# Kernel tuning notes

Measured on AMD Instinct MI355X. Metric: run time of the kernel, lower is better.

## Reference

```python
import jax, jax.numpy as jnp
import numpy as np

B, T, D, HS = 4, 4096, 1024, 64

def setup_inputs() -> dict:
    key = jax.random.key(0)
    kx, kq, kk, kv = jax.random.split(key, 4)
    s = 1.0 / np.sqrt(D)  # torch Linear default-ish init scale
    return {
        "x": jax.random.normal(kx, (B, T, D), dtype=jnp.float32),
        "Wq": jax.random.uniform(kq, (D, HS), jnp.float32, -s, s),
        "Wk": jax.random.uniform(kk, (D, HS), jnp.float32, -s, s),
        "Wv": jax.random.uniform(kv, (D, HS), jnp.float32, -s, s),
    }

def reference(x, Wq, Wk, Wv):
    # x: [B,T,D]; Wq/Wk/Wv: [D,HS]
    q = jnp.einsum('btd,dh->bth', x, Wq)
    k = jnp.einsum('btd,dh->bth', x, Wk)
    v = jnp.einsum('btd,dh->bth', x, Wv)
    # NOTE: source scales by C**-0.5 with C = d_model (input dim), not head_size
    scale = jnp.asarray(D, x.dtype) ** -0.5
    weights = jnp.einsum('bqh,bkh->bqk', q, k) * scale  # [B,T,T]
    weights = jax.nn.softmax(weights, axis=-1)
    out = jnp.einsum('bqk,bkh->bqh', weights, v)  # [B,T,HS]
    return out
```

## Files before the change

kernel.cpp:

```cpp
#include <hip/hip_runtime.h>


typedef __bf16 bf16;
typedef __bf16 bf16x4 __attribute__((ext_vector_type(4)));
typedef __bf16 bf16x8 __attribute__((ext_vector_type(8)));
typedef float  f32x16 __attribute__((ext_vector_type(16)));

#define MFMA(a, b, c) __builtin_amdgcn_mfma_f32_32x32x16_bf16(a, b, c, 0, 0, 0)

constexpr int T = 4096, D = 1024, HS = 64;
constexpr int ROWS = 4 * T;
constexpr float QSCL = 0.045084220027797f;

__device__ __forceinline__ void gld16(const void* g, void* l) {
    __builtin_amdgcn_global_load_lds(
        (const __attribute__((address_space(1))) unsigned int*)g,
        (__attribute__((address_space(3))) unsigned int*)l, 16, 0, 0);
}

__device__ inline f32x16 zero16() {
    f32x16 z;
#pragma unroll
    for (int i = 0; i < 16; ++i) z[i] = 0.f;
    return z;
}

__global__ __launch_bounds__(256) void prep_wt(
    const float* __restrict__ Wq, const float* __restrict__ Wk,
    const float* __restrict__ Wv, bf16* __restrict__ Wt)
{
    __shared__ float Xf[64 * 68];
    const int m = blockIdx.x >> 4, dt = blockIdx.x & 15;
    const float* W = (m == 0) ? Wq : ((m == 1) ? Wk : Wv);
    const int d0 = dt * 64;
#pragma unroll
    for (int j = 0; j < 4; ++j) {
        int i = threadIdx.x + 256 * j;
        int dr = i >> 4, c4 = i & 15;
        float4 v = *(const float4*)(W + (size_t)(d0 + dr) * 64 + c4 * 4);
        *(float4*)&Xf[dr * 68 + c4 * 4] = v;
    }
    __syncthreads();
    const float scl = (m == 0) ? QSCL : 1.0f;
#pragma unroll
    for (int j = 0; j < 4; ++j) {
        int o = threadIdx.x + 256 * j;
        int h = o >> 4, dc = o & 15;
        bf16x4 w;
#pragma unroll
        for (int k = 0; k < 4; ++k) w[k] = (bf16)(Xf[(dc * 4 + k) * 68 + h] * scl);
        *(bf16x4*)(Wt + (size_t)(m * 64 + h) * D + d0 + dc * 4) = w;
    }
}

__global__ __launch_bounds__(256) void qkv_proj(
    const float* __restrict__ x, const bf16* __restrict__ Wt,
    bf16* __restrict__ Qg, bf16* __restrict__ Kgt, bf16* __restrict__ Vgt)
{
    __shared__ __align__(16) bf16  Xb[2][64 * 64];
    __shared__ __align__(16) short Ws[2][192 * 64];
    const int tid = threadIdx.x;
    const int w = tid >> 6, lane = tid & 63, ln5 = lane & 31, hi = lane >> 5;
    const int tt = w & 1, hh = w >> 1;
    const int xcd = blockIdx.x & 7, mlocal = blockIdx.x >> 3;
    const int r0 = (xcd * 32 + mlocal) * 64;
    const int wb = tid & 448;

    auto stageW = [&](int kc, int buf) {
#pragma unroll
        for (int k2 = 0; k2 < 6; ++k2) {
            int s = k2 * 256 + tid;
            int h = s >> 3, j = s & 7, u = j ^ (h & 7);
            gld16(Wt + (size_t)h * D + kc * 64 + u * 8,
                  &Ws[buf][(k2 * 256 + wb) * 8]);
        }
    };
    float4 xra[2], xrb[2];
    auto stageX_load = [&](int kc) {
#pragma unroll
        for (int k = 0; k < 2; ++k) {
            int e = k * 256 + tid;
            int r = e >> 3, d0 = (e & 7) * 8;
            const float* src = x + (size_t)(r0 + r) * D + kc * 64 + d0;
            xra[k] = *(const float4*)src;
            xrb[k] = *(const float4*)(src + 4);
        }
    };
    auto stageX_write = [&](int buf) {
#pragma unroll
        for (int k = 0; k < 2; ++k) {
            int e = k * 256 + tid;
            int r = e >> 3, d0 = (e & 7) * 8;
            bf16x8 v;
            v[0] = (bf16)xra[k].x; v[1] = (bf16)xra[k].y;
            v[2] = (bf16)xra[k].z; v[3] = (bf16)xra[k].w;
            v[4] = (bf16)xrb[k].x; v[5] = (bf16)xrb[k].y;
            v[6] = (bf16)xrb[k].z; v[7] = (bf16)xrb[k].w;
            *(bf16x8*)&Xb[buf][r * 64 + (((d0 >> 3) ^ (r & 7)) * 8)] = v;
        }
    };

    f32x16 acc0 = zero16(), acc1 = zero16(), acc2 = zero16();
    const int rx = tt * 32 + ln5;
    const int hq = hh * 32 + ln5;
    const int swz = ln5 & 7;

    stageX_load(0); stageW(0, 0); stageX_write(0);
    __syncthreads();
    for (int kc = 0; kc < 16; ++kc) {
        const int cur = kc & 1;
        if (kc < 15) { stageW(kc + 1, cur ^ 1); stageX_load(kc + 1); }
        const bf16*  Xc = &Xb[cur][0];
        const short* Wb = &Ws[cur][0];
#pragma unroll
        for (int ks = 0; ks < 4; ++ks) {
            int g = (ks * 2 + hi) ^ swz;
            bf16x8 fx = *(const bf16x8*)&Xc[rx * 64 + g * 8];
            bf16x8 w0 = *(const bf16x8*)&Wb[(hq)       * 64 + g * 8];
            bf16x8 w1 = *(const bf16x8*)&Wb[(64 + hq)  * 64 + g * 8];
            bf16x8 w2 = *(const bf16x8*)&Wb[(128 + hq) * 64 + g * 8];
            acc0 = MFMA(w0, fx, acc0);
            acc1 = MFMA(w1, fx, acc1);
            acc2 = MFMA(fx, w2, acc2);
        }
        if (kc < 15) stageX_write(cur ^ 1);
        __syncthreads();
    }

    {
        int t = r0 + tt * 32 + ln5;
#pragma unroll
        for (int g = 0; g < 4; ++g) {
            int h0 = hh * 32 + 8 * g + 4 * hi;
            bf16x4 v;
#pragma unroll
            for (int k = 0; k < 4; ++k) v[k] = (bf16)acc0[4 * g + k];
            *(bf16x4*)(Qg + (size_t)t * HS + h0) = v;
        }
    }
    {
        int t = r0 + tt * 32 + ln5;
#pragma unroll
        for (int g = 0; g < 4; ++g) {
            int h0 = hh * 32 + 8 * g + 4 * hi;
            bf16x4 v;
#pragma unroll
            for (int k = 0; k < 4; ++k) v[k] = (bf16)acc1[4 * g + k];
            int j = (h0 >> 3) ^ (t & 7);
            *(bf16x4*)(Kgt + (size_t)t * HS + j * 8 + 4 * hi) = v;
        }
    }
    {
        int hr = hh * 32 + ln5;
#pragma unroll
        for (int g = 0; g < 4; ++g) {
            int t0 = tt * 32 + 8 * g + 4 * hi;
            bf16x4 v;
#pragma unroll
            for (int k = 0; k < 4; ++k) v[k] = (bf16)acc2[4 * g + k];
            int j = (t0 >> 3) ^ (hr & 7);
            *(bf16x4*)(Vgt + (size_t)r0 * HS + hr * 64 + j * 8 + 4 * hi) = v;
        }
    }
}

__global__ __launch_bounds__(256, 2) void attn(
    const bf16* __restrict__ Qg, const bf16* __restrict__ Kgt,
    const bf16* __restrict__ Vgt, float* __restrict__ Op,
    float* __restrict__ Lp, float* __restrict__ out, int split)
{
    __shared__ __align__(16) short PO[16384];
    __shared__ float Lx[128];

    const int tid = threadIdx.x;
    const int w = tid >> 6, lane = tid & 63, ln5 = lane & 31, hi = lane >> 5;
    const int wq = w & 1, wk = w >> 1;

    int b, qt, half;
    if (split == 4) {
        int rest = blockIdx.x >> 3; qt = rest & 31;
        int combo = (blockIdx.x & 7) + 8 * (rest >> 5);
        b = combo >> 2; half = combo & 3;
    } else if (split == 2) {
        int c2 = blockIdx.x & 7; b = c2 >> 1; half = c2 & 1; qt = blockIdx.x >> 3;
    } else { b = blockIdx.x & 3; half = 0; qt = blockIdx.x >> 2; }

    const int rbase = b * T;
    const int seg = T / split;
    const int kb0 = rbase + half * seg;
    const int nc = seg / 64;
    const int qrow0 = rbase + qt * 128 + wq * 64;

    bf16x8 bq[2][4];
    {
        const bf16* qp = Qg + (size_t)(qrow0 + ln5) * HS + hi * 8;
#pragma unroll
        for (int qs = 0; qs < 2; ++qs)
#pragma unroll
            for (int ks = 0; ks < 4; ++ks)
                bq[qs][ks] = *(const bf16x8*)(qp + (size_t)qs * 32 * HS + ks * 16);
    }

    const bf16* Kc = Kgt + (size_t)kb0 * HS;
    const bf16* Vc = Vgt + (size_t)kb0 * HS;

    f32x16 O00 = zero16(), O01 = zero16(), O10 = zero16(), O11 = zero16();
    float l0 = 0.f, l1 = 0.f;
    const int swz = ln5 & 7;
    const int krow = (wk * 32 + ln5) * 64;
    const int ko0 = krow + ((0 + hi) ^ swz) * 8;
    const int ko1 = krow + ((2 + hi) ^ swz) * 8;
    const int ko2 = krow + ((4 + hi) ^ swz) * 8;
    const int ko3 = krow + ((6 + hi) ^ swz) * 8;
    const int ku0 = ((wk * 4 + 0 + hi) ^ swz) * 8;
    const int ku1 = ((wk * 4 + 2 + hi) ^ swz) * 8;
    const int vr0 = ln5 * 64, vr1 = (32 + ln5) * 64;

    bf16x8 kf0 = *(const bf16x8*)(Kc + ko0);
    bf16x8 kf1 = *(const bf16x8*)(Kc + ko1);
    bf16x8 kf2 = *(const bf16x8*)(Kc + ko2);
    bf16x8 kf3 = *(const bf16x8*)(Kc + ko3);

    union U8 { unsigned u[4]; bf16x8 v; };

    for (int c = 0; c < nc; ++c) {
        const bf16* Vb = Vc + (size_t)c * 4096;
        bf16x8 v00 = *(const bf16x8*)(Vb + vr0 + ku0);
        bf16x8 v01 = *(const bf16x8*)(Vb + vr0 + ku1);
        bf16x8 v10 = *(const bf16x8*)(Vb + vr1 + ku0);
        bf16x8 v11 = *(const bf16x8*)(Vb + vr1 + ku1);
        const bool pf = (c + 1 < nc);
        bf16x8 kn0, kn1, kn2, kn3;
        if (pf) {
            const bf16* Kn = Kc + (size_t)(c + 1) * 4096;
            kn0 = *(const bf16x8*)(Kn + ko0);
            kn1 = *(const bf16x8*)(Kn + ko1);
            kn2 = *(const bf16x8*)(Kn + ko2);
            kn3 = *(const bf16x8*)(Kn + ko3);
        }

        f32x16 S0 = zero16(), S1 = zero16();
        __builtin_amdgcn_s_setprio(1);
        S0 = MFMA(kf0, bq[0][0], S0); S1 = MFMA(kf0, bq[1][0], S1);
        S0 = MFMA(kf1, bq[0][1], S0); S1 = MFMA(kf1, bq[1][1], S1);
        S0 = MFMA(kf2, bq[0][2], S0); S1 = MFMA(kf2, bq[1][2], S1);
        S0 = MFMA(kf3, bq[0][3], S0); S1 = MFMA(kf3, bq[1][3], S1);
        __builtin_amdgcn_s_setprio(0);

        unsigned wa[8], wbq[8];
#pragma unroll
        for (int g = 0; g < 4; ++g) {
            float p0 = __builtin_amdgcn_exp2f(S0[4 * g + 0]);
            float p1 = __builtin_amdgcn_exp2f(S0[4 * g + 1]);
            float p2 = __builtin_amdgcn_exp2f(S0[4 * g + 2]);
            float p3 = __builtin_amdgcn_exp2f(S0[4 * g + 3]);
            l0 += (p0 + p1) + (p2 + p3);
            asm("v_cvt_pk_bf16_f32 %0, %1, %2" : "=v"(wa[2 * g])     : "v"(p0), "v"(p1));
            asm("v_cvt_pk_bf16_f32 %0, %1, %2" : "=v"(wa[2 * g + 1]) : "v"(p2), "v"(p3));
        }
#pragma unroll
        for (int g = 0; g < 4; ++g) {
            float p0 = __builtin_amdgcn_exp2f(S1[4 * g + 0]);
            float p1 = __builtin_amdgcn_exp2f(S1[4 * g + 1]);
            float p2 = __builtin_amdgcn_exp2f(S1[4 * g + 2]);
            float p3 = __builtin_amdgcn_exp2f(S1[4 * g + 3]);
            l1 += (p0 + p1) + (p2 + p3);
            asm("v_cvt_pk_bf16_f32 %0, %1, %2" : "=v"(wbq[2 * g])     : "v"(p0), "v"(p1));
            asm("v_cvt_pk_bf16_f32 %0, %1, %2" : "=v"(wbq[2 * g + 1]) : "v"(p2), "v"(p3));
        }
#pragma unroll
        for (int j = 0; j < 2; ++j) {
            asm("v_permlane32_swap_b32 %0, %1" : "+v"(wa[j]),      "+v"(wa[j + 2]));
            asm("v_permlane32_swap_b32 %0, %1" : "+v"(wa[4 + j]),  "+v"(wa[6 + j]));
            asm("v_permlane32_swap_b32 %0, %1" : "+v"(wbq[j]),     "+v"(wbq[j + 2]));
            asm("v_permlane32_swap_b32 %0, %1" : "+v"(wbq[4 + j]), "+v"(wbq[6 + j]));
        }
        U8 fa0, fa1, fb0, fb1;
        fa0.u[0] = wa[0];  fa0.u[1] = wa[1];  fa0.u[2] = wa[2];  fa0.u[3] = wa[3];
        fa1.u[0] = wa[4];  fa1.u[1] = wa[5];  fa1.u[2] = wa[6];  fa1.u[3] = wa[7];
        fb0.u[0] = wbq[0]; fb0.u[1] = wbq[1]; fb0.u[2] = wbq[2]; fb0.u[3] = wbq[3];
        fb1.u[0] = wbq[4]; fb1.u[1] = wbq[5]; fb1.u[2] = wbq[6]; fb1.u[3] = wbq[7];

        __builtin_amdgcn_s_setprio(1);
        O00 = MFMA(v00, fa0.v, O00);
        O01 = MFMA(v00, fb0.v, O01);
        O10 = MFMA(v10, fa0.v, O10);
        O11 = MFMA(v10, fb0.v, O11);
        O00 = MFMA(v01, fa1.v, O00);
        O01 = MFMA(v01, fb1.v, O01);
        O10 = MFMA(v11, fa1.v, O10);
        O11 = MFMA(v11, fb1.v, O11);
        __builtin_amdgcn_s_setprio(0);

        if (pf) { kf0 = kn0; kf1 = kn1; kf2 = kn2; kf3 = kn3; }
    }

    l0 += __shfl_xor(l0, 32, 64);
    l1 += __shfl_xor(l1, 32, 64);

    __syncthreads();
    float* Ox = (float*)&PO[0];
    if (wk == 1) {
#pragma unroll
        for (int g = 0; g < 4; ++g)
#pragma unroll
            for (int k = 0; k < 4; ++k) {
                int h0 = 8 * g + 4 * hi + k;
                Ox[wq * 4096 + h0 * 64 + ln5]             = O00[4 * g + k];
                Ox[wq * 4096 + h0 * 64 + 32 + ln5]        = O01[4 * g + k];
                Ox[wq * 4096 + (32 + h0) * 64 + ln5]      = O10[4 * g + k];
                Ox[wq * 4096 + (32 + h0) * 64 + 32 + ln5] = O11[4 * g + k];
            }
        if (hi == 0) { Lx[wq * 64 + ln5] = l0; Lx[wq * 64 + 32 + ln5] = l1; }
    }
    __syncthreads();
    if (wk == 0) {
#pragma unroll
        for (int g = 0; g < 4; ++g)
#pragma unroll
            for (int k = 0; k < 4; ++k) {
                int h0 = 8 * g + 4 * hi + k;
                O00[4 * g + k] += Ox[wq * 4096 + h0 * 64 + ln5];
                O01[4 * g + k] += Ox[wq * 4096 + h0 * 64 + 32 + ln5];
                O10[4 * g + k] += Ox[wq * 4096 + (32 + h0) * 64 + ln5];
                O11[4 * g + k] += Ox[wq * 4096 + (32 + h0) * 64 + 32 + ln5];
            }
        l0 += Lx[wq * 64 + ln5];
        l1 += Lx[wq * 64 + 32 + ln5];

        int q0 = qrow0 + ln5, q1 = qrow0 + 32 + ln5;
        if (split == 1) {
            float i0 = 1.0f / l0, i1 = 1.0f / l1;
#pragma unroll
            for (int g = 0; g < 4; ++g) {
                int h0 = 8 * g + 4 * hi;
                float4 o;
                o.x = O00[4*g+0]*i0; o.y = O00[4*g+1]*i0; o.z = O00[4*g+2]*i0; o.w = O00[4*g+3]*i0;
                *(float4*)(out + (size_t)q0 * HS + h0) = o;
                o.x = O01[4*g+0]*i1; o.y = O01[4*g+1]*i1; o.z = O01[4*g+2]*i1; o.w = O01[4*g+3]*i1;
                *(float4*)(out + (size_t)q1 * HS + h0) = o;
                o.x = O10[4*g+0]*i0; o.y = O10[4*g+1]*i0; o.z = O10[4*g+2]*i0; o.w = O10[4*g+3]*i0;
                *(float4*)(out + (size_t)q0 * HS + 32 + h0) = o;
                o.x = O11[4*g+0]*i1; o.y = O11[4*g+1]*i1; o.z = O11[4*g+2]*i1; o.w = O11[4*g+3]*i1;
                *(float4*)(out + (size_t)q1 * HS + 32 + h0) = o;
            }
        } else {
            float* Od = Op + (size_t)half * ROWS * HS;
#pragma unroll
            for (int g = 0; g < 4; ++g) {
                int h0 = 8 * g + 4 * hi;
                float4 o;
                o.x = O00[4*g+0]; o.y = O00[4*g+1]; o.z = O00[4*g+2]; o.w = O00[4*g+3];
                *(float4*)(Od + (size_t)q0 * HS + h0) = o;
                o.x = O01[4*g+0]; o.y = O01[4*g+1]; o.z = O01[4*g+2]; o.w = O01[4*g+3];
                *(float4*)(Od + (size_t)q1 * HS + h0) = o;
                o.x = O10[4*g+0]; o.y = O10[4*g+1]; o.z = O10[4*g+2]; o.w = O10[4*g+3];
                *(float4*)(Od + (size_t)q0 * HS + 32 + h0) = o;
                o.x = O11[4*g+0]; o.y = O11[4*g+1]; o.z = O11[4*g+2]; o.w = O11[4*g+3];
                *(float4*)(Od + (size_t)q1 * HS + 32 + h0) = o;
            }
            if (hi == 0) {
                Lp[half * ROWS + q0] = l0;
                Lp[half * ROWS + q1] = l1;
            }
        }
    }
}

__global__ __launch_bounds__(256) void attn_reduce(
    const float* __restrict__ Op, const float* __restrict__ Lp,
    float* __restrict__ out, int split)
{
    int idx = blockIdx.x * 256 + threadIdx.x;
    int row = idx >> 4;
    float4 s; s.x = s.y = s.z = s.w = 0.f;
    float lsum = 0.f;
    for (int h = 0; h < split; ++h) {
        float4 a = *(const float4*)(Op + (size_t)h * ROWS * HS + (size_t)idx * 4);
        s.x += a.x; s.y += a.y; s.z += a.z; s.w += a.w;
        lsum += Lp[h * ROWS + row];
    }
    float inv = 1.0f / lsum;
    s.x *= inv; s.y *= inv; s.z *= inv; s.w *= inv;
    *(float4*)(out + (size_t)idx * 4) = s;
}

extern "C" void kernel_launch(void* const* d_in, const int* in_sizes, int n_in,
                              void* d_out, int out_size, void* d_ws, size_t ws_size,
                              hipStream_t stream)
{
    const float* x  = (const float*)d_in[0];
    const float* Wq = (const float*)d_in[1];
    const float* Wk = (const float*)d_in[2];
    const float* Wv = (const float*)d_in[3];
    float* out = (float*)d_out;

    char* ws = (char*)d_ws;
    bf16* Qg  = (bf16*)(ws);
    bf16* Kgt = (bf16*)(ws + ((size_t)2 << 20));
    bf16* Vgt = (bf16*)(ws + ((size_t)4 << 20));
    bf16* Wt  = (bf16*)(ws + ((size_t)6 << 20));
    float* Lp = (float*)(ws + ((size_t)6 << 20));
    float* Op = (float*)(ws + ((size_t)6 << 20) + ((size_t)1 << 19));

    const size_t base = ((size_t)6 << 20) + ((size_t)1 << 19);
    int split = 1;
    if (ws_size >= base + (size_t)4 * ROWS * HS * sizeof(float)) split = 4;
    else if (ws_size >= base + (size_t)2 * ROWS * HS * sizeof(float)) split = 2;

    prep_wt<<<48, 256, 0, stream>>>(Wq, Wk, Wv, Wt);
    qkv_proj<<<256, 256, 0, stream>>>(x, Wt, Qg, Kgt, Vgt);
    attn<<<128 * split, 256, 0, stream>>>(Qg, Kgt, Vgt, Op, Lp, out, split);
    if (split > 1)
        attn_reduce<<<(ROWS * HS / 4) / 256, 256, 0, stream>>>(Op, Lp, out, split);
}
```

Before: 143.2 us.

## Software-pipeline QK MFMA of next chunk with softmax and PV of current

Unrolls the attention loop by two and issues the QK^T MFMAs for the next key chunk before the exp/convert/permute and PV MFMAs of the current chunk. The goal is to let matrix-core work overlap the transcendental and VALU softmax work, hiding the dependency between score computation and probability use. It keeps an extra set of score accumulators and K fragments live, which raises register pressure. It also assumes the chunk count is even, since the loop steps by two and always loads the second chunk.

Result: slower. 171.2 us (+19.5%).

```diff
diff --git a/kernel.cpp b/kernel.cpp
--- a/kernel.cpp
+++ b/kernel.cpp
@@ -216,37 +216,20 @@
     const int ku1 = ((wk * 4 + 2 + hi) ^ swz) * 8;
     const int vr0 = ln5 * 64, vr1 = (32 + ln5) * 64;
 
-    bf16x8 kf0 = *(const bf16x8*)(Kc + ko0);
-    bf16x8 kf1 = *(const bf16x8*)(Kc + ko1);
-    bf16x8 kf2 = *(const bf16x8*)(Kc + ko2);
-    bf16x8 kf3 = *(const bf16x8*)(Kc + ko3);
-
     union U8 { unsigned u[4]; bf16x8 v; };
 
-    for (int c = 0; c < nc; ++c) {
-        const bf16* Vb = Vc + (size_t)c * 4096;
-        bf16x8 v00 = *(const bf16x8*)(Vb + vr0 + ku0);
-        bf16x8 v01 = *(const bf16x8*)(Vb + vr0 + ku1);
-        bf16x8 v10 = *(const bf16x8*)(Vb + vr1 + ku0);
-        bf16x8 v11 = *(const bf16x8*)(Vb + vr1 + ku1);
-        const bool pf = (c + 1 < nc);
-        bf16x8 kn0, kn1, kn2, kn3;
-        if (pf) {
-            const bf16* Kn = Kc + (size_t)(c + 1) * 4096;
-            kn0 = *(const bf16x8*)(Kn + ko0);
-            kn1 = *(const bf16x8*)(Kn + ko1);
-            kn2 = *(const bf16x8*)(Kn + ko2);
-            kn3 = *(const bf16x8*)(Kn + ko3);
-        }
-
-        f32x16 S0 = zero16(), S1 = zero16();
+    auto qk = [&](bf16x8 k0, bf16x8 k1, bf16x8 k2, bf16x8 k3,
+                  f32x16& S0, f32x16& S1) {
+        S0 = zero16(); S1 = zero16();
         __builtin_amdgcn_s_setprio(1);
-        S0 = MFMA(kf0, bq[0][0], S0); S1 = MFMA(kf0, bq[1][0], S1);
-        S0 = MFMA(kf1, bq[0][1], S0); S1 = MFMA(kf1, bq[1][1], S1);
-        S0 = MFMA(kf2, bq[0][2], S0); S1 = MFMA(kf2, bq[1][2], S1);
-        S0 = MFMA(kf3, bq[0][3], S0); S1 = MFMA(kf3, bq[1][3], S1);
+        S0 = MFMA(k0, bq[0][0], S0); S1 = MFMA(k0, bq[1][0], S1);
+        S0 = MFMA(k1, bq[0][1], S0); S1 = MFMA(k1, bq[1][1], S1);
+        S0 = MFMA(k2, bq[0][2], S0); S1 = MFMA(k2, bq[1][2], S1);
+        S0 = MFMA(k3, bq[0][3], S0); S1 = MFMA(k3, bq[1][3], S1);
         __builtin_amdgcn_s_setprio(0);
-
+    };
+    auto sm = [&](const f32x16& S0, const f32x16& S1,
+                  U8& fa0, U8& fa1, U8& fb0, U8& fb1) {
         unsigned wa[8], wbq[8];
 #pragma unroll
         for (int g = 0; g < 4; ++g) {
@@ -275,12 +258,13 @@
             asm("v_permlane32_swap_b32 %0, %1" : "+v"(wbq[j]),     "+v"(wbq[j + 2]));
             asm("v_permlane32_swap_b32 %0, %1" : "+v"(wbq[4 + j]), "+v"(wbq[6 + j]));
         }
-        U8 fa0, fa1, fb0, fb1;
         fa0.u[0] = wa[0];  fa0.u[1] = wa[1];  fa0.u[2] = wa[2];  fa0.u[3] = wa[3];
         fa1.u[0] = wa[4];  fa1.u[1] = wa[5];  fa1.u[2] = wa[6];  fa1.u[3] = wa[7];
         fb0.u[0] = wbq[0]; fb0.u[1] = wbq[1]; fb0.u[2] = wbq[2]; fb0.u[3] = wbq[3];
         fb1.u[0] = wbq[4]; fb1.u[1] = wbq[5]; fb1.u[2] = wbq[6]; fb1.u[3] = wbq[7];
-
+    };
+    auto pv = [&](bf16x8 v00, bf16x8 v01, bf16x8 v10, bf16x8 v11,
+                  const U8& fa0, const U8& fa1, const U8& fb0, const U8& fb1) {
         __builtin_amdgcn_s_setprio(1);
         O00 = MFMA(v00, fa0.v, O00);
         O01 = MFMA(v00, fb0.v, O01);
@@ -291,8 +275,58 @@
         O10 = MFMA(v11, fa1.v, O10);
         O11 = MFMA(v11, fb1.v, O11);
         __builtin_amdgcn_s_setprio(0);
-
-        if (pf) { kf0 = kn0; kf1 = kn1; kf2 = kn2; kf3 = kn3; }
+    };
+
+    bf16x8 kA0 = *(const bf16x8*)(Kc + ko0);
+    bf16x8 kA1 = *(const bf16x8*)(Kc + ko1);
+    bf16x8 kA2 = *(const bf16x8*)(Kc + ko2);
+    bf16x8 kA3 = *(const bf16x8*)(Kc + ko3);
+    f32x16 SA0, SA1;
+    qk(kA0, kA1, kA2, kA3, SA0, SA1);
+    bf16x8 kB0 = *(const bf16x8*)(Kc + 4096 + ko0);
+    bf16x8 kB1 = *(const bf16x8*)(Kc + 4096 + ko1);
+    bf16x8 kB2 = *(const bf16x8*)(Kc + 4096 + ko2);
+    bf16x8 kB3 = *(const bf16x8*)(Kc + 4096 + ko3);
+
+    for (int c = 0; c < nc; c += 2) {
+        const bool p2 = (c + 2 < nc);
+        const bf16* VbA = Vc + (size_t)c * 4096;
+        bf16x8 vA00 = *(const bf16x8*)(VbA + vr0 + ku0);
+        bf16x8 vA01 = *(const bf16x8*)(VbA + vr0 + ku1);
+        bf16x8 vA10 = *(const bf16x8*)(VbA + vr1 + ku0);
+        bf16x8 vA11 = *(const bf16x8*)(VbA + vr1 + ku1);
+        if (p2) {
+            const bf16* Kn = Kc + (size_t)(c + 2) * 4096;
+            kA0 = *(const bf16x8*)(Kn + ko0);
+            kA1 = *(const bf16x8*)(Kn + ko1);
+            kA2 = *(const bf16x8*)(Kn + ko2);
+            kA3 = *(const bf16x8*)(Kn + ko3);
+        }
+        f32x16 SB0, SB1;
+        qk(kB0, kB1, kB2, kB3, SB0, SB1);
+        {
+            U8 fa0, fa1, fb0, fb1;
+            sm(SA0, SA1, fa0, fa1, fb0, fb1);
+            pv(vA00, vA01, vA10, vA11, fa0, fa1, fb0, fb1);
+        }
+        const bf16* VbB = VbA + 4096;
+        bf16x8 vB00 = *(const bf16x8*)(VbB + vr0 + ku0);
+        bf16x8 vB01 = *(const bf16x8*)(VbB + vr0 + ku1);
+        bf16x8 vB10 = *(const bf16x8*)(VbB + vr1 + ku0);
+        bf16x8 vB11 = *(const bf16x8*)(VbB + vr1 + ku1);
+        if (p2) {
+            const bf16* Kn = Kc + (size_t)(c + 3) * 4096;
+            kB0 = *(const bf16x8*)(Kn + ko0);
+            kB1 = *(const bf16x8*)(Kn + ko1);
+            kB2 = *(const bf16x8*)(Kn + ko2);
+            kB3 = *(const bf16x8*)(Kn + ko3);
+        }
+        if (p2) qk(kA0, kA1, kA2, kA3, SA0, SA1);
+        {
+            U8 fa0, fa1, fb0, fb1;
+            sm(SB0, SB1, fa0, fa1, fb0, fb1);
+            pv(vB00, vB01, vB10, vB11, fa0, fa1, fb0, fb1);
+        }
     }
 
     l0 += __shfl_xor(l0, 32, 64);
```
